# Performance work log

Measured on AMD Instinct MI355X. Metric: run time of the kernel, lower is better.

Reference implementation:

```python
import jax, jax.numpy as jnp
import numpy as np

VOCAB, EMB, H = 50000, 300, 64  # fgian_config: embed_dim=300, hidden_dim=64
POL = 3


def _lstm(x, lens, Wih, Whh, b):
    """Masked unidirectional LSTM (PyTorch gate order i,f,g,o).
    x: [B,T,D]; outputs zero past each sequence's length (packed-LSTM semantics)."""
    B, T, _ = x.shape
    Hh = Whh.shape[1]
    xs = jnp.einsum('btd,gd->btg', x, Wih) + b  # precompute input projection [B,T,4H]

    def step(carry, inp):
        h, c = carry
        xproj, t = inp
        g = xproj + h @ Whh.T
        i, f, gg, o = jnp.split(g, 4, axis=-1)
        i = jax.nn.sigmoid(i); f = jax.nn.sigmoid(f)
        gg = jnp.tanh(gg); o = jax.nn.sigmoid(o)
        c_new = f * c + i * gg
        h_new = o * jnp.tanh(c_new)
        m = (t < lens)[:, None]
        return (jnp.where(m, h_new, h), jnp.where(m, c_new, c)), jnp.where(m, h_new, 0.0)

    h0 = jnp.zeros((B, Hh), x.dtype)
    _, out = jax.lax.scan(step, (h0, h0), (xs.transpose(1, 0, 2), jnp.arange(T)))
    return out.transpose(1, 0, 2)


def _bilstm(x, lens, Wih_f, Whh_f, b_f, Wih_b, Whh_b, b_b):
    B, T, _ = x.shape
    t = jnp.arange(T)
    fwd = _lstm(x, lens, Wih_f, Whh_f, b_f)
    # reverse each sequence within its valid length, run fwd scan, reverse back
    ridx = jnp.clip(lens[:, None] - 1 - t[None, :], 0)  # [B,T]
    x_rev = jnp.take_along_axis(x, ridx[..., None], axis=1)
    bwd_rev = _lstm(x_rev, lens, Wih_b, Whh_b, b_b)
    bwd = jnp.take_along_axis(bwd_rev, ridx[..., None], axis=1)
    bwd = jnp.where((t[None, :] < lens[:, None])[..., None], bwd, 0.0)
    return jnp.concatenate([fwd, bwd], axis=-1)  # [B,T,2H]


def setup_inputs() -> dict:
    key = jax.random.key(0)
    ks = jax.random.split(key, 20)
    s = 0.1
    d = {
        'body_idx': jax.random.randint(ks[0], (128, 512), 0, VOCAB),
        'pun_idx': jax.random.randint(ks[1], (128, 256), 0, VOCAB),
        'emb': jax.random.normal(ks[2], (VOCAB, EMB), jnp.float32) * s,
        'w_u': jax.random.normal(ks[15], (6 * H,), jnp.float32) * s,
        'Wd': jax.random.normal(ks[16], (POL, 4 * H), jnp.float32) * s,
        'bd': jnp.zeros((POL,), jnp.float32),
    }
    names = ['bWih_f', 'bWhh_f', 'bb_f', 'bWih_b', 'bWhh_b', 'bb_b',
             'pWih_f', 'pWhh_f', 'pb_f', 'pWih_b', 'pWhh_b', 'pb_b']
    shapes = [(4 * H, EMB), (4 * H, H), (4 * H,)] * 4
    for i, (n, sh) in enumerate(zip(names, shapes)):
        d[n] = jax.random.normal(ks[3 + i], sh, jnp.float32) * s
    return d


def reference(body_idx, pun_idx, emb,
              bWih_f, bWhh_f, bb_f, bWih_b, bWhh_b, bb_b,
              pWih_f, pWhh_f, pb_f, pWih_b, pWhh_b, pb_b,
              w_u, Wd, bd):
    body_len = jnp.sum(body_idx != 0, axis=1)
    pun_len = jnp.sum(pun_idx != 0, axis=1)
    body_M = _bilstm(emb[body_idx], body_len, bWih_f, bWhh_f, bb_f, bWih_b, bWhh_b, bb_b)  # [B,T,2H]
    pun_M = _bilstm(emb[pun_idx], pun_len, pWih_f, pWhh_f, pb_f, pWih_b, pWhh_b, pb_b)     # [B,P,2H]

    # alignment[b,i,j] = [body_i, pun_j, body_i*pun_j] . w_u  -> fully vectorized
    w1, w2, w3 = jnp.split(w_u, 3)
    align = (jnp.einsum('btd,d->bt', body_M, w1)[:, :, None]
             + jnp.einsum('bpd,d->bp', pun_M, w2)[:, None, :]
             + jnp.einsum('btd,bpd->btp', body_M * w3, pun_M))  # [B,T,P]

    att_b = jax.nn.softmax(align.max(axis=2), axis=1)  # [B,T]
    f_pun2body = jnp.einsum('btd,bt->bd', body_M, att_b)
    att_p = jax.nn.softmax(align.max(axis=1), axis=1)  # [B,P]
    f_body2pun = jnp.einsum('bp,bpd->bd', att_p, pun_M)

    feat = jnp.concatenate([f_pun2body, f_body2pun], axis=1)  # [B,4H]
    return feat @ Wd.T + bd
```

## Files before the change

kernel.cpp:

```cpp
#include <hip/hip_runtime.h>


#define B 128
#define TBODY 512
#define TPUN 256
#define EMB 300
#define EMBP 320
#define VOCAB 50000
#define HID 64
#define G4 256
#define NG 512
#define DM 128

typedef __attribute__((ext_vector_type(8))) short bf16x8;
typedef __attribute__((ext_vector_type(4))) float floatx4;
typedef unsigned short u16;

#define OFF_XPB   0u
#define OFF_XPP   134217728u
#define OFF_BODYM 201326592u
#define OFF_PUNM  234881024u
#define OFF_SMALL 251658240u
#define OFF_ABODY (OFF_XPB + 0u)
#define OFF_APUN  (OFF_XPB + 262144u)
#define OFF_MT    (OFF_XPB + 393216u)
#define OFF_MP    (OFF_XPB + 655360u)
#define OFF_COLP  (OFF_XPB + 786432u)
#define OFF_EMBB  OFF_BODYM
#define OFF_WCB   OFF_PUNM
#define OFF_WCP   (OFF_PUNM + 327680u)
#define OFF_BIASB (OFF_PUNM + 655360u)
#define OFF_BIASP (OFF_PUNM + 657408u)
#define OFF_LENS  OFF_SMALL
#define OFF_FEAT  (OFF_SMALL + 1024u)

__device__ inline u16 f2bf(float v) {
    unsigned int u = __float_as_uint(v);
    unsigned int r = (u + 0x7FFFu + ((u >> 16) & 1u)) >> 16;
    return (u16)r;
}

__device__ inline void gload_lds16(const void* g, void* l) {
    __builtin_amdgcn_global_load_lds(
        (const __attribute__((address_space(1))) unsigned int*)g,
        (__attribute__((address_space(3))) unsigned int*)l, 16, 0, 0);
}

#define QBC(v, gg) __int_as_float(__builtin_amdgcn_update_dpp( \
    0, __float_as_int(v), (gg) * 0x55, 0xF, 0xF, true))

__global__ __launch_bounds__(256) void k_lens(const int* __restrict__ bidx,
                                              const int* __restrict__ pidx,
                                              int* __restrict__ lens) {
    int j = blockIdx.x, tid = threadIdx.x;
    const int* src; int n;
    if (j < B) { src = bidx + (size_t)j * TBODY; n = TBODY; }
    else       { src = pidx + (size_t)(j - B) * TPUN; n = TPUN; }
    int c = 0;
    for (int t = tid; t < n; t += 256) c += (src[t] != 0) ? 1 : 0;
    for (int o = 32; o; o >>= 1) c += __shfl_xor(c, o, 64);
    __shared__ int red[4];
    if ((tid & 63) == 0) red[tid >> 6] = c;
    __syncthreads();
    if (tid == 0) lens[j] = red[0] + red[1] + red[2] + red[3];
}

__global__ __launch_bounds__(256) void k_prep_emb(const float* __restrict__ emb,
                                                  u16* __restrict__ embb) {
    int e = blockIdx.x * 256 + threadIdx.x;
    int row = e / EMBP, d = e - row * EMBP;
    float v = (d < EMB) ? emb[(size_t)row * EMB + d] : 0.f;
    embb[e] = f2bf(v);
}

__global__ __launch_bounds__(256) void k_prep_w(
    const float* __restrict__ bWih_f, const float* __restrict__ bWih_b,
    const float* __restrict__ bb_f, const float* __restrict__ bb_b,
    const float* __restrict__ pWih_f, const float* __restrict__ pWih_b,
    const float* __restrict__ pb_f, const float* __restrict__ pb_b,
    u16* __restrict__ Wcb, u16* __restrict__ Wcp,
    float* __restrict__ biasb, float* __restrict__ biasp) {
    int e = blockIdx.x * 256 + threadIdx.x;
    const int WSZ = NG * EMBP;
    if (e < WSZ) {
        int g = e / EMBP, d = e - g * EMBP;
        float v = 0.f;
        if (d < EMB) v = (g < G4) ? bWih_f[g * EMB + d] : bWih_b[(g - G4) * EMB + d];
        Wcb[e] = f2bf(v);
    } else if (e < 2 * WSZ) {
        int ee = e - WSZ;
        int g = ee / EMBP, d = ee - g * EMBP;
        float v = 0.f;
        if (d < EMB) v = (g < G4) ? pWih_f[g * EMB + d] : pWih_b[(g - G4) * EMB + d];
        Wcp[ee] = f2bf(v);
    } else if (e < 2 * WSZ + NG) {
        int g = e - 2 * WSZ;
        biasb[g] = (g < G4) ? bb_f[g] : bb_b[g - G4];
    } else if (e < 2 * WSZ + 2 * NG) {
        int g = e - 2 * WSZ - NG;
        biasp[g] = (g < G4) ? pb_f[g] : pb_b[g - G4];
    }
}

__global__ __launch_bounds__(256) void k_gemm(const int* __restrict__ idx,
                                              const u16* __restrict__ embb,
                                              const u16* __restrict__ Wc,
                                              const float* __restrict__ biasc,
                                              float* __restrict__ out) {
    __shared__ u16 As[128 * 32];
    __shared__ u16 Bs[128 * 32];
    int tid = threadIdx.x, wave = tid >> 6, lane = tid & 63;
    int m0 = blockIdx.x * 128, g0 = blockIdx.y * 128;

    const u16* agp[2]; const u16* bgp[2];
    u16* asd[2]; u16* bsd[2];
#pragma unroll
    for (int j = 0; j < 2; j++) {
        int rbase = wave * 32 + j * 16;
        int r = rbase + (lane >> 2);
        int clog = (lane & 3) ^ (r & 3);
        int arow = idx[m0 + r];
        agp[j] = embb + (size_t)arow * EMBP + clog * 8;
        bgp[j] = Wc + (size_t)(g0 + r) * EMBP + clog * 8;
        asd[j] = As + rbase * 32;
        bsd[j] = Bs + rbase * 32;
    }

    int l15 = lane & 15, quad = lane >> 4;
    int mt0 = (wave >> 1) * 4, nt0 = (wave & 1) * 4;
    const u16* ard[4]; const u16* brd[4];
#pragma unroll
    for (int a = 0; a < 4; a++) {
        int r = (mt0 + a) * 16 + l15;
        ard[a] = As + r * 32 + ((quad ^ (r & 3)) * 8);
        int n = (nt0 + a) * 16 + l15;
        brd[a] = Bs + n * 32 + ((quad ^ (n & 3)) * 8);
    }

    floatx4 acc[4][4];
#pragma unroll
    for (int a = 0; a < 4; a++)
#pragma unroll
        for (int c = 0; c < 4; c++) acc[a][c] = (floatx4){0.f, 0.f, 0.f, 0.f};

    for (int k0 = 0; k0 < EMBP; k0 += 32) {
#pragma unroll
        for (int j = 0; j < 2; j++) {
            gload_lds16(agp[j] + k0, asd[j]);
            gload_lds16(bgp[j] + k0, bsd[j]);
        }
        __syncthreads();
        bf16x8 af[4], bfr[4];
#pragma unroll
        for (int a = 0; a < 4; a++) { af[a] = *(const bf16x8*)ard[a]; bfr[a] = *(const bf16x8*)brd[a]; }
#pragma unroll
        for (int a = 0; a < 4; a++)
#pragma unroll
            for (int c = 0; c < 4; c++)
                acc[a][c] = __builtin_amdgcn_mfma_f32_16x16x32_bf16(af[a], bfr[c], acc[a][c], 0, 0, 0);
        __syncthreads();
    }

#pragma unroll
    for (int c = 0; c < 4; c++) {
        int gcol = g0 + (nt0 + c) * 16 + l15;
        float bv = biasc[gcol];
#pragma unroll
        for (int a = 0; a < 4; a++) {
            int row0 = m0 + (mt0 + a) * 16 + quad * 4;
#pragma unroll
            for (int rg = 0; rg < 4; rg++)
                out[(size_t)(row0 + rg) * NG + gcol] = acc[a][c][rg] + bv;
        }
    }
}

#define DECLWR(n) \
    float Wr##n##0, Wr##n##1, Wr##n##2, Wr##n##3; \
    { int qs_ = (((l16 - (n)) & 15) << 2); \
      Wr##n##0 = vw[qs_]; Wr##n##1 = vw[qs_ + 1]; \
      Wr##n##2 = vw[qs_ + 2]; Wr##n##3 = vw[qs_ + 3]; }
#define FMACD(ACC, H, W, N) \
    asm("v_fmac_f32_dpp %0, %1, %2 row_ror:" #N " row_mask:0xf bank_mask:0xf" \
        : "+v"(ACC) : "v"(H), "v"(W));
#define RORF(n) { \
    FMACD(a0, hq.x, Wr##n##0, n) FMACD(a1, hq.y, Wr##n##1, n) \
    FMACD(a2, hq.z, Wr##n##2, n) FMACD(a3, hq.w, Wr##n##3, n) }

#define SBODY(S, XR) { \
    int p_ = dir ? (len - 1 - (S)) : (S); \
    float xv = XR; \
    int pn_ = dir ? (len - 3 - (S)) : ((S) + 2); \
    pn_ = min(max(pn_, 0), T - 1); \
    XR = xg[(size_t)pn_ * NG]; \
    float4 hq = *(const float4*)(&hbuf[(S) & 1][l16 * 4]); \
    float a0 = xv, a1 = 0.f, a2 = 0.f, a3 = 0.f; \
    a0 = fmaf(hq.x, Wr00, a0); a1 = fmaf(hq.y, Wr01, a1); \
    a2 = fmaf(hq.z, Wr02, a2); a3 = fmaf(hq.w, Wr03, a3); \
    RORF(1)  RORF(2)  RORF(3)  RORF(4)  RORF(5) \
    RORF(6)  RORF(7)  RORF(8)  RORF(9)  RORF(10) \
    RORF(11) RORF(12) RORF(13) RORF(14) RORF(15) \
    float pre = (a0 + a1) + (a2 + a3); \
    bool isg = (g == 2); \
    float t_in = isg ? (2.f * pre) : (-pre); \
    float e_ = __expf(t_in); \
    float r_ = __builtin_amdgcn_rcpf(1.f + e_); \
    float val = isg ? fmaf(-2.f, r_, 1.f) : r_; \
    float vi = QBC(val, 0); \
    float vf = QBC(val, 1); \
    float vg = QBC(val, 2); \
    float vo = QBC(val, 3); \
    c = fmaf(vf, c, vi * vg); \
    float th = fmaf(-2.f, __builtin_amdgcn_rcpf(1.f + __expf(2.f * c)), 1.f); \
    float h = vo * th; \
    if (g == 0) { \
        hbuf[((S) & 1) ^ 1][u] = h; \
        outp[(size_t)p_ * DM + u] = h; \
    } \
    asm volatile("s_waitcnt lgkmcnt(0)\n\ts_barrier" ::: "memory"); }

__global__ __attribute__((amdgpu_flat_work_group_size(256, 256),
                          amdgpu_waves_per_eu(2, 2))) void k_scan(
    const float* __restrict__ xpB, const float* __restrict__ xpP,
    float* __restrict__ bodyM, float* __restrict__ punM,
    const int* __restrict__ lens,
    const float* __restrict__ bWhh_f, const float* __restrict__ bWhh_b,
    const float* __restrict__ pWhh_f, const float* __restrict__ pWhh_b) {
    int task = blockIdx.x, tid = threadIdx.x;
    int isPun = task >> 8;
    int sub = task & 255;
    int b = sub & 127, dir = sub >> 7;
    int T = isPun ? TPUN : TBODY;
    int len = lens[(isPun ? B : 0) + b];
    int w = tid >> 6, l = tid & 63;
    int g = l & 3, q = l >> 2;
    int u = w * 16 + q;
    int l16 = l & 15;
    const float* xp = (isPun ? xpP : xpB) + (size_t)b * T * NG + dir * G4;
    float* outp = (isPun ? punM : bodyM) + (size_t)b * T * DM + dir * HID;
    const float* Whh = isPun ? (dir ? pWhh_b : pWhh_f) : (dir ? bWhh_b : bWhh_f);

    const volatile float* vw = Whh + (size_t)(g * 64 + u) * 64;
    DECLWR(0)  DECLWR(1)  DECLWR(2)  DECLWR(3)
    DECLWR(4)  DECLWR(5)  DECLWR(6)  DECLWR(7)
    DECLWR(8)  DECLWR(9)  DECLWR(10) DECLWR(11)
    DECLWR(12) DECLWR(13) DECLWR(14) DECLWR(15)

    __shared__ __align__(16) float hbuf[2][64];
    if (tid < 64) hbuf[0][tid] = 0.f;
    __syncthreads();
    if (len <= 0) return;

    const float* xg = xp + g * 64 + u;
    float c = 0.f;
    int p0 = dir ? (len - 1) : 0;
    int p1 = dir ? (len - 2) : 1;
    p1 = min(max(p1, 0), T - 1);
    float xA = xg[(size_t)p0 * NG];
    float xB = xg[(size_t)p1 * NG];
    int s = 0;
    for (; s + 1 < len; s += 2) {
        SBODY(s, xA)
        SBODY(s + 1, xB)
    }
    if (s < len) { SBODY(s, xA) }
}

__global__ __launch_bounds__(256) void k_rowdot(const float* __restrict__ bodyM,
                                                const float* __restrict__ punM,
                                                const float* __restrict__ w_u,
                                                float* __restrict__ a_body,
                                                float* __restrict__ a_pun) {
    int wid = (blockIdx.x * 256 + threadIdx.x) >> 6;
    int lane = threadIdx.x & 63;
    const int NB = B * TBODY;
    const float* src; const float* wv; float* dst;
    if (wid < NB) { src = bodyM + (size_t)wid * DM; wv = w_u; dst = a_body + wid; }
    else { src = punM + (size_t)(wid - NB) * DM; wv = w_u + DM; dst = a_pun + (wid - NB); }
    float2 v = ((const float2*)src)[lane];
    float2 w = ((const float2*)wv)[lane];
    float s = v.x * w.x + v.y * w.y;
    for (int o = 32; o; o >>= 1) s += __shfl_xor(s, o, 64);
    if (lane == 0) *dst = s;
}

__global__ __launch_bounds__(256) void k_align(
    const float* __restrict__ bodyM, const float* __restrict__ punM,
    const float* __restrict__ a_body, const float* __restrict__ a_pun,
    const float* __restrict__ w_u,
    float* __restrict__ m_t, float* __restrict__ colpart) {
    __shared__ float bw[64 * 132];
    __shared__ float pu[64 * 129];
    __shared__ float colred[64 * 16];
    int tid = threadIdx.x;
    int tt = blockIdx.x, b = blockIdx.y;
    int t0 = tt * 64;
    int ti = tid >> 4, pi = tid & 15;
    const float* w3 = w_u + 2 * DM;
    const float* bsrc = bodyM + ((size_t)b * TBODY + t0) * DM;
#pragma unroll
    for (int j = 0; j < 8; j++) {
        int e = tid + 256 * j;
        int i = e >> 5, c4 = e & 31;
        float4 v = *(const float4*)(bsrc + i * DM + c4 * 4);
        float4 wv = *(const float4*)(w3 + c4 * 4);
        v.x *= wv.x; v.y *= wv.y; v.z *= wv.z; v.w *= wv.w;
        *(float4*)(bw + i * 132 + c4 * 4) = v;
    }
    float aB[4];
#pragma unroll
    for (int a = 0; a < 4; a++) aB[a] = a_body[(size_t)b * TBODY + t0 + ti * 4 + a];
    float mrun[4] = {-1e30f, -1e30f, -1e30f, -1e30f};
    for (int pc = 0; pc < 4; pc++) {
        __syncthreads();
        const float* psrc = punM + ((size_t)b * TPUN + pc * 64) * DM;
#pragma unroll
        for (int j = 0; j < 8; j++) {
            int e = tid + 256 * j;
            int i = e >> 5, c4 = e & 31;
            float4 v = *(const float4*)(psrc + i * DM + c4 * 4);
            pu[i * 129 + c4 * 4 + 0] = v.x;
            pu[i * 129 + c4 * 4 + 1] = v.y;
            pu[i * 129 + c4 * 4 + 2] = v.z;
            pu[i * 129 + c4 * 4 + 3] = v.w;
        }
        __syncthreads();
        float aP[4];
#pragma unroll
        for (int c = 0; c < 4; c++) aP[c] = a_pun[(size_t)b * TPUN + pc * 64 + pi * 4 + c];
        float C[4][4];
#pragma unroll
        for (int a = 0; a < 4; a++)
#pragma unroll
            for (int c = 0; c < 4; c++) C[a][c] = 0.f;
        for (int d4 = 0; d4 < 32; d4++) {
            float4 bq[4];
#pragma unroll
            for (int a = 0; a < 4; a++) bq[a] = *(const float4*)(bw + (ti * 4 + a) * 132 + d4 * 4);
#pragma unroll
            for (int dd = 0; dd < 4; dd++) {
                float pv[4];
#pragma unroll
                for (int c = 0; c < 4; c++) pv[c] = pu[(pi * 4 + c) * 129 + d4 * 4 + dd];
#pragma unroll
                for (int a = 0; a < 4; a++) {
                    float bvv = (dd == 0) ? bq[a].x : (dd == 1) ? bq[a].y : (dd == 2) ? bq[a].z : bq[a].w;
#pragma unroll
                    for (int c = 0; c < 4; c++) C[a][c] += bvv * pv[c];
                }
            }
        }
        float colv[4] = {-1e30f, -1e30f, -1e30f, -1e30f};
#pragma unroll
        for (int a = 0; a < 4; a++) {
            float rm = -1e30f;
#pragma unroll
            for (int c = 0; c < 4; c++) {
                float valv = C[a][c] + aB[a] + aP[c];
                rm = fmaxf(rm, valv);
                colv[c] = fmaxf(colv[c], valv);
            }
#pragma unroll
            for (int o = 1; o < 16; o <<= 1) rm = fmaxf(rm, __shfl_xor(rm, o, 64));
            mrun[a] = fmaxf(mrun[a], rm);
        }
#pragma unroll
        for (int c = 0; c < 4; c++) colred[(pi * 4 + c) * 16 + ti] = colv[c];
        __syncthreads();
        if (tid < 64) {
            float m = -1e30f;
#pragma unroll
            for (int k = 0; k < 16; k++) m = fmaxf(m, colred[tid * 16 + k]);
            colpart[((size_t)b * 8 + tt) * TPUN + pc * 64 + tid] = m;
        }
    }
    if (pi == 0) {
#pragma unroll
        for (int a = 0; a < 4; a++) m_t[(size_t)b * TBODY + t0 + ti * 4 + a] = mrun[a];
    }
}

__global__ __launch_bounds__(256) void k_colmax(const float* __restrict__ colpart,
                                                float* __restrict__ m_p) {
    int b = blockIdx.x, p = threadIdx.x;
    float m = -1e30f;
    for (int tt = 0; tt < 8; tt++) m = fmaxf(m, colpart[((size_t)b * 8 + tt) * TPUN + p]);
    m_p[(size_t)b * TPUN + p] = m;
}

__global__ __launch_bounds__(256) void k_feat(const float* __restrict__ bodyM,
                                              const float* __restrict__ punM,
                                              const float* __restrict__ m_t,
                                              const float* __restrict__ m_p,
                                              float* __restrict__ feat) {
    int bidx = blockIdx.x;
    int b = bidx & (B - 1), which = bidx >> 7;
    int n = which ? TPUN : TBODY;
    const float* sc = which ? (m_p + (size_t)b * TPUN) : (m_t + (size_t)b * TBODY);
    const float* src = which ? (punM + (size_t)b * TPUN * DM) : (bodyM + (size_t)b * TBODY * DM);
    float* dst = feat + (size_t)b * 256 + which * DM;
    int tid = threadIdx.x;
    __shared__ float e_lds[TBODY];
    __shared__ float red[8];
    __shared__ float red2[256];
    float mx = -1e30f;
    for (int t = tid; t < n; t += 256) mx = fmaxf(mx, sc[t]);
    for (int o = 32; o; o >>= 1) mx = fmaxf(mx, __shfl_xor(mx, o, 64));
    if ((tid & 63) == 0) red[tid >> 6] = mx;
    __syncthreads();
    mx = fmaxf(fmaxf(red[0], red[1]), fmaxf(red[2], red[3]));
    float se = 0.f;
    for (int t = tid; t < n; t += 256) {
        float ev = __expf(sc[t] - mx);
        e_lds[t] = ev;
        se += ev;
    }
    for (int o = 32; o; o >>= 1) se += __shfl_xor(se, o, 64);
    if ((tid & 63) == 0) red[4 + (tid >> 6)] = se;
    __syncthreads();
    se = red[4] + red[5] + red[6] + red[7];
    float inv = 1.f / se;
    int d = tid & 127, half = tid >> 7;
    float acc = 0.f;
    for (int t = half; t < n; t += 2) acc += e_lds[t] * src[(size_t)t * DM + d];
    red2[tid] = acc;
    __syncthreads();
    if (tid < DM) dst[tid] = (red2[tid] + red2[tid + 128]) * inv;
}

__global__ __launch_bounds__(256) void k_out(const float* __restrict__ feat,
                                             const float* __restrict__ Wd,
                                             const float* __restrict__ bd,
                                             float* __restrict__ outp) {
    int b = blockIdx.x, tid = threadIdx.x;
    float v = feat[(size_t)b * 256 + tid];
    __shared__ float red[12];
#pragma unroll
    for (int pol = 0; pol < 3; pol++) {
        float s = v * Wd[pol * 256 + tid];
        for (int o = 32; o; o >>= 1) s += __shfl_xor(s, o, 64);
        if ((tid & 63) == 0) red[pol * 4 + (tid >> 6)] = s;
    }
    __syncthreads();
    if (tid < 3) outp[b * 3 + tid] = red[tid * 4] + red[tid * 4 + 1] + red[tid * 4 + 2] + red[tid * 4 + 3] + bd[tid];
}

extern "C" void kernel_launch(void* const* d_in, const int* in_sizes, int n_in,
                              void* d_out, int out_size, void* d_ws, size_t ws_size,
                              hipStream_t stream) {
    const int* body_idx = (const int*)d_in[0];
    const int* pun_idx  = (const int*)d_in[1];
    const float* emb    = (const float*)d_in[2];
    const float* w_u    = (const float*)d_in[3];
    const float* Wd     = (const float*)d_in[4];
    const float* bd     = (const float*)d_in[5];
    const float* bWih_f = (const float*)d_in[6];
    const float* bWhh_f = (const float*)d_in[7];
    const float* bb_f   = (const float*)d_in[8];
    const float* bWih_b = (const float*)d_in[9];
    const float* bWhh_b = (const float*)d_in[10];
    const float* bb_b   = (const float*)d_in[11];
    const float* pWih_f = (const float*)d_in[12];
    const float* pWhh_f = (const float*)d_in[13];
    const float* pb_f   = (const float*)d_in[14];
    const float* pWih_b = (const float*)d_in[15];
    const float* pWhh_b = (const float*)d_in[16];
    const float* pb_b   = (const float*)d_in[17];

    char* ws = (char*)d_ws;
    float* xpB   = (float*)(ws + OFF_XPB);
    float* xpP   = (float*)(ws + OFF_XPP);
    float* bodyM = (float*)(ws + OFF_BODYM);
    float* punM  = (float*)(ws + OFF_PUNM);
    u16* embb    = (u16*)(ws + OFF_EMBB);
    u16* Wcb     = (u16*)(ws + OFF_WCB);
    u16* Wcp     = (u16*)(ws + OFF_WCP);
    float* biasb = (float*)(ws + OFF_BIASB);
    float* biasp = (float*)(ws + OFF_BIASP);
    int* lens    = (int*)(ws + OFF_LENS);
    float* a_body = (float*)(ws + OFF_ABODY);
    float* a_pun  = (float*)(ws + OFF_APUN);
    float* m_t    = (float*)(ws + OFF_MT);
    float* m_p    = (float*)(ws + OFF_MP);
    float* colpart = (float*)(ws + OFF_COLP);
    float* feat   = (float*)(ws + OFF_FEAT);
    float* outp   = (float*)d_out;

    k_lens<<<dim3(256), dim3(256), 0, stream>>>(body_idx, pun_idx, lens);
    k_prep_emb<<<dim3(62500), dim3(256), 0, stream>>>(emb, embb);
    k_prep_w<<<dim3(1284), dim3(256), 0, stream>>>(bWih_f, bWih_b, bb_f, bb_b,
                                                   pWih_f, pWih_b, pb_f, pb_b,
                                                   Wcb, Wcp, biasb, biasp);
    k_gemm<<<dim3(512, 4), dim3(256), 0, stream>>>(body_idx, embb, Wcb, biasb, xpB);
    k_gemm<<<dim3(256, 4), dim3(256), 0, stream>>>(pun_idx, embb, Wcp, biasp, xpP);
    hipMemsetAsync(ws + OFF_BODYM, 0, (size_t)(33554432u + 16777216u), stream);
    k_scan<<<dim3(512), dim3(256), 0, stream>>>(xpB, xpP, bodyM, punM, lens,
                                                bWhh_f, bWhh_b, pWhh_f, pWhh_b);
    k_rowdot<<<dim3(24576), dim3(256), 0, stream>>>(bodyM, punM, w_u, a_body, a_pun);
    k_align<<<dim3(8, 128), dim3(256), 0, stream>>>(bodyM, punM, a_body, a_pun, w_u, m_t, colpart);
    k_colmax<<<dim3(128), dim3(256), 0, stream>>>(colpart, m_p);
    k_feat<<<dim3(256), dim3(256), 0, stream>>>(bodyM, punM, m_t, m_p, feat);
    k_out<<<dim3(128), dim3(256), 0, stream>>>(feat, Wd, bd, outp);
}
```

Baseline: 637.1 us.

## Fuse forward and backward LSTM directions into one scan block

Each scan block now runs the forward and backward recurrences of one sequence together, interleaving their two independent dependency chains. This halves the block count from 512 to 256 and shares one barrier per step across both directions, giving the scheduler more independent work to hide latency. The cost is twice the recurrent weights held in registers (waves_per_eu changed to 1) and fewer blocks to spread across the GPU's compute units.

```diff
diff --git a/kernel.cpp b/kernel.cpp
--- a/kernel.cpp
+++ b/kernel.cpp
@@ -175,95 +175,122 @@
     }
 }
 
-#define DECLWR(n) \
-    float Wr##n##0, Wr##n##1, Wr##n##2, Wr##n##3; \
+#define DECLWR(P, n) \
+    float P##n##_0, P##n##_1, P##n##_2, P##n##_3; \
     { int qs_ = (((l16 - (n)) & 15) << 2); \
-      Wr##n##0 = vw[qs_]; Wr##n##1 = vw[qs_ + 1]; \
-      Wr##n##2 = vw[qs_ + 2]; Wr##n##3 = vw[qs_ + 3]; }
+      P##n##_0 = vw##P[qs_]; P##n##_1 = vw##P[qs_ + 1]; \
+      P##n##_2 = vw##P[qs_ + 2]; P##n##_3 = vw##P[qs_ + 3]; }
 #define FMACD(ACC, H, W, N) \
     asm("v_fmac_f32_dpp %0, %1, %2 row_ror:" #N " row_mask:0xf bank_mask:0xf" \
         : "+v"(ACC) : "v"(H), "v"(W));
-#define RORF(n) { \
-    FMACD(a0, hq.x, Wr##n##0, n) FMACD(a1, hq.y, Wr##n##1, n) \
-    FMACD(a2, hq.z, Wr##n##2, n) FMACD(a3, hq.w, Wr##n##3, n) }
-
-#define SBODY(S, XR) { \
-    int p_ = dir ? (len - 1 - (S)) : (S); \
-    float xv = XR; \
-    int pn_ = dir ? (len - 3 - (S)) : ((S) + 2); \
-    pn_ = min(max(pn_, 0), T - 1); \
-    XR = xg[(size_t)pn_ * NG]; \
-    float4 hq = *(const float4*)(&hbuf[(S) & 1][l16 * 4]); \
-    float a0 = xv, a1 = 0.f, a2 = 0.f, a3 = 0.f; \
-    a0 = fmaf(hq.x, Wr00, a0); a1 = fmaf(hq.y, Wr01, a1); \
-    a2 = fmaf(hq.z, Wr02, a2); a3 = fmaf(hq.w, Wr03, a3); \
-    RORF(1)  RORF(2)  RORF(3)  RORF(4)  RORF(5) \
-    RORF(6)  RORF(7)  RORF(8)  RORF(9)  RORF(10) \
-    RORF(11) RORF(12) RORF(13) RORF(14) RORF(15) \
-    float pre = (a0 + a1) + (a2 + a3); \
-    bool isg = (g == 2); \
-    float t_in = isg ? (2.f * pre) : (-pre); \
-    float e_ = __expf(t_in); \
-    float r_ = __builtin_amdgcn_rcpf(1.f + e_); \
-    float val = isg ? fmaf(-2.f, r_, 1.f) : r_; \
-    float vi = QBC(val, 0); \
-    float vf = QBC(val, 1); \
-    float vg = QBC(val, 2); \
-    float vo = QBC(val, 3); \
-    c = fmaf(vf, c, vi * vg); \
-    float th = fmaf(-2.f, __builtin_amdgcn_rcpf(1.f + __expf(2.f * c)), 1.f); \
-    float h = vo * th; \
+#define RORF2(n) { \
+    FMACD(a0, hqA.x, A##n##_0, n) FMACD(b0, hqB.x, B##n##_0, n) \
+    FMACD(a1, hqA.y, A##n##_1, n) FMACD(b1, hqB.y, B##n##_1, n) \
+    FMACD(a2, hqA.z, A##n##_2, n) FMACD(b2, hqB.z, B##n##_2, n) \
+    FMACD(a3, hqA.w, A##n##_3, n) FMACD(b3, hqB.w, B##n##_3, n) }
+
+#define SBODY2(S, XRA, XRB) { \
+    int pA_ = (S); \
+    int pB_ = len - 1 - (S); \
+    float xvA_ = XRA, xvB_ = XRB; \
+    int pnA_ = min(max((S) + 2, 0), T - 1); \
+    int pnB_ = min(max(len - 3 - (S), 0), T - 1); \
+    XRA = xgA[(size_t)pnA_ * NG]; \
+    XRB = xgB[(size_t)pnB_ * NG]; \
+    float4 hqA = *(const float4*)(&hbuf[0][(S) & 1][l16 * 4]); \
+    float4 hqB = *(const float4*)(&hbuf[1][(S) & 1][l16 * 4]); \
+    float a0 = xvA_, a1 = 0.f, a2 = 0.f, a3 = 0.f; \
+    float b0 = xvB_, b1 = 0.f, b2 = 0.f, b3 = 0.f; \
+    a0 = fmaf(hqA.x, A0_0, a0); b0 = fmaf(hqB.x, B0_0, b0); \
+    a1 = fmaf(hqA.y, A0_1, a1); b1 = fmaf(hqB.y, B0_1, b1); \
+    a2 = fmaf(hqA.z, A0_2, a2); b2 = fmaf(hqB.z, B0_2, b2); \
+    a3 = fmaf(hqA.w, A0_3, a3); b3 = fmaf(hqB.w, B0_3, b3); \
+    RORF2(1)  RORF2(2)  RORF2(3)  RORF2(4)  RORF2(5) \
+    RORF2(6)  RORF2(7)  RORF2(8)  RORF2(9)  RORF2(10) \
+    RORF2(11) RORF2(12) RORF2(13) RORF2(14) RORF2(15) \
+    float preA_ = (a0 + a1) + (a2 + a3); \
+    float preB_ = (b0 + b1) + (b2 + b3); \
+    bool isg_ = (g == 2); \
+    float tA_ = isg_ ? (2.f * preA_) : (-preA_); \
+    float tB_ = isg_ ? (2.f * preB_) : (-preB_); \
+    float eA_ = __expf(tA_), eB_ = __expf(tB_); \
+    float rA_ = __builtin_amdgcn_rcpf(1.f + eA_); \
+    float rB_ = __builtin_amdgcn_rcpf(1.f + eB_); \
+    float valA_ = isg_ ? fmaf(-2.f, rA_, 1.f) : rA_; \
+    float valB_ = isg_ ? fmaf(-2.f, rB_, 1.f) : rB_; \
+    float viA_ = QBC(valA_, 0), vfA_ = QBC(valA_, 1); \
+    float vgA_ = QBC(valA_, 2), voA_ = QBC(valA_, 3); \
+    float viB_ = QBC(valB_, 0), vfB_ = QBC(valB_, 1); \
+    float vgB_ = QBC(valB_, 2), voB_ = QBC(valB_, 3); \
+    cA = fmaf(vfA_, cA, viA_ * vgA_); \
+    cB = fmaf(vfB_, cB, viB_ * vgB_); \
+    float thA_ = fmaf(-2.f, __builtin_amdgcn_rcpf(1.f + __expf(2.f * cA)), 1.f); \
+    float thB_ = fmaf(-2.f, __builtin_amdgcn_rcpf(1.f + __expf(2.f * cB)), 1.f); \
+    float hA_ = voA_ * thA_; \
+    float hB_ = voB_ * thB_; \
     if (g == 0) { \
-        hbuf[((S) & 1) ^ 1][u] = h; \
-        outp[(size_t)p_ * DM + u] = h; \
+        hbuf[0][((S) & 1) ^ 1][u] = hA_; \
+        hbuf[1][((S) & 1) ^ 1][u] = hB_; \
+        outpA[(size_t)pA_ * DM + u] = hA_; \
+        outpB[(size_t)pB_ * DM + u] = hB_; \
     } \
     asm volatile("s_waitcnt lgkmcnt(0)\n\ts_barrier" ::: "memory"); }
 
 __global__ __attribute__((amdgpu_flat_work_group_size(256, 256),
-                          amdgpu_waves_per_eu(2, 2))) void k_scan(
+                          amdgpu_waves_per_eu(1, 1))) void k_scan(
     const float* __restrict__ xpB, const float* __restrict__ xpP,
     float* __restrict__ bodyM, float* __restrict__ punM,
     const int* __restrict__ lens,
     const float* __restrict__ bWhh_f, const float* __restrict__ bWhh_b,
     const float* __restrict__ pWhh_f, const float* __restrict__ pWhh_b) {
     int task = blockIdx.x, tid = threadIdx.x;
-    int isPun = task >> 8;
-    int sub = task & 255;
-    int b = sub & 127, dir = sub >> 7;
+    int isPun = task >> 7;
+    int b = task & 127;
     int T = isPun ? TPUN : TBODY;
     int len = lens[(isPun ? B : 0) + b];
     int w = tid >> 6, l = tid & 63;
     int g = l & 3, q = l >> 2;
     int u = w * 16 + q;
     int l16 = l & 15;
-    const float* xp = (isPun ? xpP : xpB) + (size_t)b * T * NG + dir * G4;
-    float* outp = (isPun ? punM : bodyM) + (size_t)b * T * DM + dir * HID;
-    const float* Whh = isPun ? (dir ? pWhh_b : pWhh_f) : (dir ? bWhh_b : bWhh_f);
-
-    const volatile float* vw = Whh + (size_t)(g * 64 + u) * 64;
-    DECLWR(0)  DECLWR(1)  DECLWR(2)  DECLWR(3)
-    DECLWR(4)  DECLWR(5)  DECLWR(6)  DECLWR(7)
-    DECLWR(8)  DECLWR(9)  DECLWR(10) DECLWR(11)
-    DECLWR(12) DECLWR(13) DECLWR(14) DECLWR(15)
-
-    __shared__ __align__(16) float hbuf[2][64];
-    if (tid < 64) hbuf[0][tid] = 0.f;
+    const float* xbase = (isPun ? xpP : xpB) + (size_t)b * T * NG;
+    float* Mbase = (isPun ? punM : bodyM) + (size_t)b * T * DM;
+    float* outpA = Mbase;
+    float* outpB = Mbase + HID;
+    const float* WhhA = isPun ? pWhh_f : bWhh_f;
+    const float* WhhB = isPun ? pWhh_b : bWhh_b;
+
+    const volatile float* vwA = WhhA + (size_t)(g * 64 + u) * 64;
+    const volatile float* vwB = WhhB + (size_t)(g * 64 + u) * 64;
+    DECLWR(A, 0)  DECLWR(A, 1)  DECLWR(A, 2)  DECLWR(A, 3)
+    DECLWR(A, 4)  DECLWR(A, 5)  DECLWR(A, 6)  DECLWR(A, 7)
+    DECLWR(A, 8)  DECLWR(A, 9)  DECLWR(A, 10) DECLWR(A, 11)
+    DECLWR(A, 12) DECLWR(A, 13) DECLWR(A, 14) DECLWR(A, 15)
+    DECLWR(B, 0)  DECLWR(B, 1)  DECLWR(B, 2)  DECLWR(B, 3)
+    DECLWR(B, 4)  DECLWR(B, 5)  DECLWR(B, 6)  DECLWR(B, 7)
+    DECLWR(B, 8)  DECLWR(B, 9)  DECLWR(B, 10) DECLWR(B, 11)
+    DECLWR(B, 12) DECLWR(B, 13) DECLWR(B, 14) DECLWR(B, 15)
+
+    __shared__ __align__(16) float hbuf[2][2][64];
+    if (tid < 128) hbuf[tid >> 6][0][tid & 63] = 0.f;
     __syncthreads();
     if (len <= 0) return;
 
-    const float* xg = xp + g * 64 + u;
-    float c = 0.f;
-    int p0 = dir ? (len - 1) : 0;
-    int p1 = dir ? (len - 2) : 1;
-    p1 = min(max(p1, 0), T - 1);
-    float xA = xg[(size_t)p0 * NG];
-    float xB = xg[(size_t)p1 * NG];
+    const float* xgA = xbase + g * 64 + u;
+    const float* xgB = xbase + G4 + g * 64 + u;
+    float cA = 0.f, cB = 0.f;
+    int pA1 = min(max(1, 0), T - 1);
+    int pB0 = len - 1;
+    int pB1 = min(max(len - 2, 0), T - 1);
+    float xAe = xgA[0];
+    float xAo = xgA[(size_t)pA1 * NG];
+    float xBe = xgB[(size_t)pB0 * NG];
+    float xBo = xgB[(size_t)pB1 * NG];
     int s = 0;
     for (; s + 1 < len; s += 2) {
-        SBODY(s, xA)
-        SBODY(s + 1, xB)
-    }
-    if (s < len) { SBODY(s, xA) }
+        SBODY2(s, xAe, xBe)
+        SBODY2(s + 1, xAo, xBo)
+    }
+    if (s < len) { SBODY2(s, xAe, xBe) }
 }
 
 __global__ __launch_bounds__(256) void k_rowdot(const float* __restrict__ bodyM,
@@ -494,7 +521,7 @@
     k_gemm<<<dim3(512, 4), dim3(256), 0, stream>>>(body_idx, embb, Wcb, biasb, xpB);
     k_gemm<<<dim3(256, 4), dim3(256), 0, stream>>>(pun_idx, embb, Wcp, biasp, xpP);
     hipMemsetAsync(ws + OFF_BODYM, 0, (size_t)(33554432u + 16777216u), stream);
-    k_scan<<<dim3(512), dim3(256), 0, stream>>>(xpB, xpP, bodyM, punM, lens,
+    k_scan<<<dim3(256), dim3(256), 0, stream>>>(xpB, xpP, bodyM, punM, lens,
                                                 bWhh_f, bWhh_b, pWhh_f, pWhh_b);
     k_rowdot<<<dim3(24576), dim3(256), 0, stream>>>(bodyM, punM, w_u, a_body, a_pun);
     k_align<<<dim3(8, 128), dim3(256), 0, stream>>>(bodyM, punM, a_body, a_pun, w_u, m_t, colpart);
```

Result: slower. 710.0 us (+11.4%).

## Process two sequences per LSTM scan block to interleave independent recurrences

Applied to the files above, without the earlier changes.

Each scan workgroup now runs two batch elements at once in the same direction, sharing the register-resident recurrent weights and interleaving the two DPP-based matvecs and gate computations. The grid halves from 512 to 256 blocks, which matches the CU count more closely, and occupancy is set to one wave per EU. The aim is to give the latency-bound sequential recurrence more independent instructions per step so that DPP and transcendental latency is hidden. In exchange, each block runs until the longer of its two sequences finishes, and the extra state raises register pressure.

```diff
diff --git a/kernel.cpp b/kernel.cpp
--- a/kernel.cpp
+++ b/kernel.cpp
@@ -183,61 +183,92 @@
 #define FMACD(ACC, H, W, N) \
     asm("v_fmac_f32_dpp %0, %1, %2 row_ror:" #N " row_mask:0xf bank_mask:0xf" \
         : "+v"(ACC) : "v"(H), "v"(W));
-#define RORF(n) { \
-    FMACD(a0, hq.x, Wr##n##0, n) FMACD(a1, hq.y, Wr##n##1, n) \
-    FMACD(a2, hq.z, Wr##n##2, n) FMACD(a3, hq.w, Wr##n##3, n) }
-
-#define SBODY(S, XR) { \
-    int p_ = dir ? (len - 1 - (S)) : (S); \
-    float xv = XR; \
-    int pn_ = dir ? (len - 3 - (S)) : ((S) + 2); \
-    pn_ = min(max(pn_, 0), T - 1); \
-    XR = xg[(size_t)pn_ * NG]; \
-    float4 hq = *(const float4*)(&hbuf[(S) & 1][l16 * 4]); \
-    float a0 = xv, a1 = 0.f, a2 = 0.f, a3 = 0.f; \
-    a0 = fmaf(hq.x, Wr00, a0); a1 = fmaf(hq.y, Wr01, a1); \
-    a2 = fmaf(hq.z, Wr02, a2); a3 = fmaf(hq.w, Wr03, a3); \
-    RORF(1)  RORF(2)  RORF(3)  RORF(4)  RORF(5) \
-    RORF(6)  RORF(7)  RORF(8)  RORF(9)  RORF(10) \
-    RORF(11) RORF(12) RORF(13) RORF(14) RORF(15) \
-    float pre = (a0 + a1) + (a2 + a3); \
-    bool isg = (g == 2); \
-    float t_in = isg ? (2.f * pre) : (-pre); \
-    float e_ = __expf(t_in); \
-    float r_ = __builtin_amdgcn_rcpf(1.f + e_); \
-    float val = isg ? fmaf(-2.f, r_, 1.f) : r_; \
-    float vi = QBC(val, 0); \
-    float vf = QBC(val, 1); \
-    float vg = QBC(val, 2); \
-    float vo = QBC(val, 3); \
-    c = fmaf(vf, c, vi * vg); \
-    float th = fmaf(-2.f, __builtin_amdgcn_rcpf(1.f + __expf(2.f * c)), 1.f); \
-    float h = vo * th; \
+#define RORF2(n) { \
+    FMACD(a0, hq0.x, Wr##n##0, n) FMACD(b0v, hq1.x, Wr##n##0, n) \
+    FMACD(a1, hq0.y, Wr##n##1, n) FMACD(b1v, hq1.y, Wr##n##1, n) \
+    FMACD(a2, hq0.z, Wr##n##2, n) FMACD(b2v, hq1.z, Wr##n##2, n) \
+    FMACD(a3, hq0.w, Wr##n##3, n) FMACD(b3v, hq1.w, Wr##n##3, n) }
+
+#define SBODY2(S, XR0, XR1) { \
+    float xv0_ = XR0, xv1_ = XR1; \
+    int pn0_ = dir ? (len0 - 3 - (S)) : ((S) + 2); \
+    pn0_ = min(max(pn0_, 0), T - 1); \
+    XR0 = xg0[(size_t)pn0_ * NG]; \
+    int pn1_ = dir ? (len1 - 3 - (S)) : ((S) + 2); \
+    pn1_ = min(max(pn1_, 0), T - 1); \
+    XR1 = xg1[(size_t)pn1_ * NG]; \
+    float4 hq0 = *(const float4*)(&hbuf[0][(S) & 1][l16 * 4]); \
+    float4 hq1 = *(const float4*)(&hbuf[1][(S) & 1][l16 * 4]); \
+    float a0 = xv0_, a1 = 0.f, a2 = 0.f, a3 = 0.f; \
+    float b0v = xv1_, b1v = 0.f, b2v = 0.f, b3v = 0.f; \
+    a0 = fmaf(hq0.x, Wr00, a0); b0v = fmaf(hq1.x, Wr00, b0v); \
+    a1 = fmaf(hq0.y, Wr01, a1); b1v = fmaf(hq1.y, Wr01, b1v); \
+    a2 = fmaf(hq0.z, Wr02, a2); b2v = fmaf(hq1.z, Wr02, b2v); \
+    a3 = fmaf(hq0.w, Wr03, a3); b3v = fmaf(hq1.w, Wr03, b3v); \
+    RORF2(1)  RORF2(2)  RORF2(3)  RORF2(4)  RORF2(5) \
+    RORF2(6)  RORF2(7)  RORF2(8)  RORF2(9)  RORF2(10) \
+    RORF2(11) RORF2(12) RORF2(13) RORF2(14) RORF2(15) \
+    float pre0_ = (a0 + a1) + (a2 + a3); \
+    float pre1_ = (b0v + b1v) + (b2v + b3v); \
+    bool isg_ = (g == 2); \
+    float t0_ = isg_ ? (2.f * pre0_) : (-pre0_); \
+    float t1_ = isg_ ? (2.f * pre1_) : (-pre1_); \
+    float e0_ = __expf(t0_), e1_ = __expf(t1_); \
+    float r0_ = __builtin_amdgcn_rcpf(1.f + e0_); \
+    float r1_ = __builtin_amdgcn_rcpf(1.f + e1_); \
+    float val0_ = isg_ ? fmaf(-2.f, r0_, 1.f) : r0_; \
+    float val1_ = isg_ ? fmaf(-2.f, r1_, 1.f) : r1_; \
+    float vi0_ = QBC(val0_, 0), vf0_ = QBC(val0_, 1); \
+    float vg0_ = QBC(val0_, 2), vo0_ = QBC(val0_, 3); \
+    float vi1_ = QBC(val1_, 0), vf1_ = QBC(val1_, 1); \
+    float vg1_ = QBC(val1_, 2), vo1_ = QBC(val1_, 3); \
+    c0 = fmaf(vf0_, c0, vi0_ * vg0_); \
+    c1 = fmaf(vf1_, c1, vi1_ * vg1_); \
+    float th0_ = fmaf(-2.f, __builtin_amdgcn_rcpf(1.f + __expf(2.f * c0)), 1.f); \
+    float th1_ = fmaf(-2.f, __builtin_amdgcn_rcpf(1.f + __expf(2.f * c1)), 1.f); \
+    float h0_ = vo0_ * th0_; \
+    float h1_ = vo1_ * th1_; \
     if (g == 0) { \
-        hbuf[((S) & 1) ^ 1][u] = h; \
-        outp[(size_t)p_ * DM + u] = h; \
+        hbuf[0][((S) & 1) ^ 1][u] = h0_; \
+        hbuf[1][((S) & 1) ^ 1][u] = h1_; \
+        if ((S) < len0) { \
+            int p0_ = dir ? (len0 - 1 - (S)) : (S); \
+            outp0[(size_t)p0_ * DM + u] = h0_; \
+        } \
+        if ((S) < len1) { \
+            int p1_ = dir ? (len1 - 1 - (S)) : (S); \
+            outp1[(size_t)p1_ * DM + u] = h1_; \
+        } \
     } \
     asm volatile("s_waitcnt lgkmcnt(0)\n\ts_barrier" ::: "memory"); }
 
 __global__ __attribute__((amdgpu_flat_work_group_size(256, 256),
-                          amdgpu_waves_per_eu(2, 2))) void k_scan(
+                          amdgpu_waves_per_eu(1, 1))) void k_scan(
     const float* __restrict__ xpB, const float* __restrict__ xpP,
     float* __restrict__ bodyM, float* __restrict__ punM,
     const int* __restrict__ lens,
     const float* __restrict__ bWhh_f, const float* __restrict__ bWhh_b,
     const float* __restrict__ pWhh_f, const float* __restrict__ pWhh_b) {
     int task = blockIdx.x, tid = threadIdx.x;
-    int isPun = task >> 8;
-    int sub = task & 255;
-    int b = sub & 127, dir = sub >> 7;
+    int isPun = task >> 7;
+    int sub = task & 127;
+    int dir = sub >> 6;
+    int bp = sub & 63;
+    int b0i = bp * 2, b1i = bp * 2 + 1;
     int T = isPun ? TPUN : TBODY;
-    int len = lens[(isPun ? B : 0) + b];
+    int len0 = lens[(isPun ? B : 0) + b0i];
+    int len1 = lens[(isPun ? B : 0) + b1i];
+    int lenM = max(len0, len1);
     int w = tid >> 6, l = tid & 63;
     int g = l & 3, q = l >> 2;
     int u = w * 16 + q;
     int l16 = l & 15;
-    const float* xp = (isPun ? xpP : xpB) + (size_t)b * T * NG + dir * G4;
-    float* outp = (isPun ? punM : bodyM) + (size_t)b * T * DM + dir * HID;
+    const float* xpS = isPun ? xpP : xpB;
+    float* MS = isPun ? punM : bodyM;
+    const float* xg0 = xpS + (size_t)b0i * T * NG + dir * G4 + g * 64 + u;
+    const float* xg1 = xpS + (size_t)b1i * T * NG + dir * G4 + g * 64 + u;
+    float* outp0 = MS + (size_t)b0i * T * DM + dir * HID;
+    float* outp1 = MS + (size_t)b1i * T * DM + dir * HID;
     const float* Whh = isPun ? (dir ? pWhh_b : pWhh_f) : (dir ? bWhh_b : bWhh_f);
 
     const volatile float* vw = Whh + (size_t)(g * 64 + u) * 64;
@@ -246,24 +277,26 @@
     DECLWR(8)  DECLWR(9)  DECLWR(10) DECLWR(11)
     DECLWR(12) DECLWR(13) DECLWR(14) DECLWR(15)
 
-    __shared__ __align__(16) float hbuf[2][64];
-    if (tid < 64) hbuf[0][tid] = 0.f;
+    __shared__ __align__(16) float hbuf[2][2][64];
+    if (tid < 128) hbuf[tid >> 6][0][tid & 63] = 0.f;
     __syncthreads();
-    if (len <= 0) return;
-
-    const float* xg = xp + g * 64 + u;
-    float c = 0.f;
-    int p0 = dir ? (len - 1) : 0;
-    int p1 = dir ? (len - 2) : 1;
-    p1 = min(max(p1, 0), T - 1);
-    float xA = xg[(size_t)p0 * NG];
-    float xB = xg[(size_t)p1 * NG];
+    if (lenM <= 0) return;
+
+    float c0 = 0.f, c1 = 0.f;
+    int q0e = dir ? (len0 - 1) : 0;  q0e = min(max(q0e, 0), T - 1);
+    int q0o = dir ? (len0 - 2) : 1;  q0o = min(max(q0o, 0), T - 1);
+    int q1e = dir ? (len1 - 1) : 0;  q1e = min(max(q1e, 0), T - 1);
+    int q1o = dir ? (len1 - 2) : 1;  q1o = min(max(q1o, 0), T - 1);
+    float x0e = xg0[(size_t)q0e * NG];
+    float x0o = xg0[(size_t)q0o * NG];
+    float x1e = xg1[(size_t)q1e * NG];
+    float x1o = xg1[(size_t)q1o * NG];
     int s = 0;
-    for (; s + 1 < len; s += 2) {
-        SBODY(s, xA)
-        SBODY(s + 1, xB)
-    }
-    if (s < len) { SBODY(s, xA) }
+    for (; s + 1 < lenM; s += 2) {
+        SBODY2(s, x0e, x1e)
+        SBODY2(s + 1, x0o, x1o)
+    }
+    if (s < lenM) { SBODY2(s, x0e, x1e) }
 }
 
 __global__ __launch_bounds__(256) void k_rowdot(const float* __restrict__ bodyM,
@@ -494,7 +527,7 @@
     k_gemm<<<dim3(512, 4), dim3(256), 0, stream>>>(body_idx, embb, Wcb, biasb, xpB);
     k_gemm<<<dim3(256, 4), dim3(256), 0, stream>>>(pun_idx, embb, Wcp, biasp, xpP);
     hipMemsetAsync(ws + OFF_BODYM, 0, (size_t)(33554432u + 16777216u), stream);
-    k_scan<<<dim3(512), dim3(256), 0, stream>>>(xpB, xpP, bodyM, punM, lens,
+    k_scan<<<dim3(256), dim3(256), 0, stream>>>(xpB, xpP, bodyM, punM, lens,
                                                 bWhh_f, bWhh_b, pWhh_f, pWhh_b);
     k_rowdot<<<dim3(24576), dim3(256), 0, stream>>>(bodyM, punM, w_u, a_body, a_pun);
     k_align<<<dim3(8, 128), dim3(256), 0, stream>>>(bodyM, punM, a_body, a_pun, w_u, m_t, colpart);
```

New measurement: 717.5 us. 12.6% more time.
